# Performance work log

Hardware: AMD Instinct MI355X
Metric: run time of the kernel (lower is better)

## Reference

```python
import jax, jax.numpy as jnp
import numpy as np

B, S, V = 512, 256, 10      # batch, s_node_num, v_node_num
E, H = 128, 128             # embedding, lstm hidden
D = 2 * H                   # num_directions * hidden
PENALTY = 1.0e6
STD = 0.1


def _cell(x, h, c, Wih, Whh, b):
    # PyTorch LSTM cell, gate order i, f, g, o; b = b_ih + b_hh
    g = x @ Wih.T + h @ Whh.T + b
    i, f, gg, o = jnp.split(g, 4, axis=-1)
    c = jax.nn.sigmoid(f) * c + jax.nn.sigmoid(i) * jnp.tanh(gg)
    h = jax.nn.sigmoid(o) * jnp.tanh(c)
    return h, c


def setup_inputs() -> dict:
    key = jax.random.key(0)
    ks = jax.random.split(key, 25)
    w = lambda k, shp: (jax.random.normal(k, shp, jnp.float32) * STD)
    return {
        's_node_indexes': jax.random.randint(ks[0], (B, S), 0, S, dtype=jnp.int32),
        's_inputs': jax.random.uniform(ks[1], (B, S, 3), jnp.float32),
        'v_input': jax.random.uniform(ks[2], (V, 3), jnp.float32) * 0.5,
        'W_embed': w(ks[3], (E, 1)),
        'enc_Wih_f': w(ks[4], (4 * H, E)), 'enc_Whh_f': w(ks[5], (4 * H, H)), 'enc_b_f': w(ks[6], (4 * H,)),
        'enc_Wih_b': w(ks[7], (4 * H, E)), 'enc_Whh_b': w(ks[8], (4 * H, H)), 'enc_b_b': w(ks[9], (4 * H,)),
        'dec_Wih_f': w(ks[10], (4 * H, D)), 'dec_Whh_f': w(ks[11], (4 * H, H)), 'dec_b_f': w(ks[12], (4 * H,)),
        'dec_Wih_b': w(ks[13], (4 * H, D)), 'dec_Whh_b': w(ks[14], (4 * H, H)), 'dec_b_b': w(ks[15], (4 * H,)),
        'W_ref': w(ks[16], (D, D)), 'W_q': w(ks[17], (D, D)), 'v_w': w(ks[18], (D,)),
        'W_ref2': w(ks[19], (D, D)), 'W_q2': w(ks[20], (D, D)), 'v2_w': w(ks[21], (D,)),
    }


def reference(s_node_indexes, s_inputs, v_input, W_embed,
              enc_Wih_f, enc_Whh_f, enc_b_f, enc_Wih_b, enc_Whh_b, enc_b_b,
              dec_Wih_f, dec_Whh_f, dec_b_f, dec_Wih_b, dec_Whh_b, dec_b_b,
              W_ref, W_q, v_w, W_ref2, W_q2, v2_w):
    Bn, Sn = s_node_indexes.shape
    # Embed: snode resource -> Linear(1, E, bias=False)
    emb = s_inputs[:, :, 0:1] @ W_embed.T            # (B, S, E)
    xs = jnp.swapaxes(emb, 0, 1)                     # (S, B, E)
    h0 = jnp.zeros((Bn, H), jnp.float32)
    c0 = jnp.zeros((Bn, H), jnp.float32)

    def enc_scan(Wih, Whh, b, seq):
        def step(carry, x):
            h, c = carry
            h, c = _cell(x, h, c, Wih, Whh, b)
            return (h, c), h
        (hT, cT), hs = jax.lax.scan(step, (h0, c0), seq)
        return hs, hT, cT

    hs_f, hf, cf = enc_scan(enc_Wih_f, enc_Whh_f, enc_b_f, xs)
    hs_b, hb, cb = enc_scan(enc_Wih_b, enc_Whh_b, enc_b_b, xs[::-1])
    Enc = jnp.swapaxes(jnp.concatenate([hs_f, hs_b[::-1]], axis=-1), 0, 1)  # (B, S, D)
    h_state = jnp.stack([hf, hb])                    # (2, B, H)
    c_state = jnp.stack([cf, cb])

    refE = Enc @ W_ref.T                             # (B, S, D) precomputed (dropout p=0)
    ref2E = Enc @ W_ref2.T

    def dec_step(carry, vcpu):
        dec_in, h, c, played = carry                 # dec_in (B, D)
        hf_, cf_ = _cell(dec_in, h[0], c[0], dec_Wih_f, dec_Whh_f, dec_b_f)
        hb_, cb_ = _cell(dec_in, h[1], c[1], dec_Wih_b, dec_Whh_b, dec_b_b)
        dec_out = jnp.concatenate([hf_, hb_], axis=-1)                       # (B, D)
        cannot = (s_inputs[:, :, 0] < vcpu).astype(jnp.float32) + played     # (B, S)
        ow = jnp.tanh(refE + (dec_out @ W_q.T)[:, None, :]) @ v_w - PENALTY * cannot
        att = jax.nn.softmax(jnp.tanh(ref2E + (dec_in @ W_q2.T)[:, None, :]) @ v2_w, axis=1)
        new_in = jnp.einsum('bs,bsd->bd', att, Enc)
        sel = jnp.argmax(ow, axis=1)
        played = played + jax.nn.one_hot(sel, Sn, dtype=jnp.float32)
        return (new_in, jnp.stack([hf_, hb_]), jnp.stack([cf_, cb_]), played), (ow, sel)

    init = (jnp.zeros((Bn, D), jnp.float32), h_state, c_state, jnp.zeros((Bn, Sn), jnp.float32))
    _, (output_weights, sels) = jax.lax.scan(dec_step, init, v_input[:, 0])
    shuffled = sels.T                                # (B, V)
    original = jnp.take_along_axis(s_node_indexes, shuffled, axis=1)
    return original, shuffled, output_weights        # output_weights: (V, B, S)
```

## Files before the change

kernel.cpp:

```cpp
#include <hip/hip_runtime.h>
#include <math.h>

#define cB 512
#define cS 256
#define cV 10
#define cE 128
#define cH 128
#define cD 256
#define cG 512
#define PEN 1.0e6f
#define S1 224
#define PADK 40

typedef _Float16 half8_t __attribute__((ext_vector_type(8)));
typedef _Float16 half4_t __attribute__((ext_vector_type(4)));
typedef float f32x4 __attribute__((ext_vector_type(4)));

#define DOT4(acc, wv, hv)                                   \
    do {                                                    \
        acc = fmaf((wv).x, (hv).x, acc);                    \
        acc = fmaf((wv).y, (hv).y, acc);                    \
        acc = fmaf((wv).z, (hv).z, acc);                    \
        acc = fmaf((wv).w, (hv).w, acc);                    \
    } while (0)

__device__ __forceinline__ float sigmf(float x) { return 1.0f / (1.0f + expf(-x)); }

__global__ void k_uprep(const float* __restrict__ Wih_f, const float* __restrict__ Wih_b,
                        const float* __restrict__ W_embed, float* __restrict__ uvec)
{
    const int j = threadIdx.x;
    const float* __restrict__ Wih = blockIdx.x ? Wih_b : Wih_f;
    float u = 0.f;
#pragma unroll 8
    for (int e = 0; e < cE; ++e) u = fmaf(Wih[(size_t)j * cE + e], W_embed[e], u);
    uvec[blockIdx.x * cG + j] = u;
}

__global__ __launch_bounds__(1024, 4) void k_encoder(
    const float* __restrict__ s_inputs, const float* __restrict__ uvec,
    const float* __restrict__ Whh_f, const float* __restrict__ b_f,
    const float* __restrict__ Whh_b, const float* __restrict__ b_b,
    _Float16* __restrict__ Ehi, _Float16* __restrict__ Elo,
    float* __restrict__ h_state, float* __restrict__ c_state)
{
    const int dir = blockIdx.x >> 7;
    const int b0  = (blockIdx.x & 127) * 4;
    const float* __restrict__ Whh = dir ? Whh_b : Whh_f;
    const float* __restrict__ bv  = dir ? b_b   : b_f;
    const int tid = threadIdx.x;
    const int j = tid & 511;
    const int hf = tid >> 9;

    __shared__ __align__(16) float a_in[4][cS];
    __shared__ __align__(16) float hbuf[4][cH];
    __shared__ __align__(16) float gpart[4][2][516];

    a_in[tid >> 8][tid & 255] =
        s_inputs[((size_t)(b0 + (tid >> 8)) * cS + (tid & 255)) * 3];

    float4 w[16];
#pragma unroll
    for (int kk = 0; kk < 16; ++kk)
        w[kk] = *(const float4*)&Whh[(size_t)j * cH + hf * 64 + kk * 4];

    const float uj = (hf == 0) ? uvec[dir * cG + j] : 0.f;
    const float bj = (hf == 0) ? bv[j] : 0.f;

    const int ur = tid >> 7, uk = tid & 127;
    float c_reg = 0.f, h_last = 0.f;
    if (tid < 512) hbuf[ur][uk] = 0.f;
    __syncthreads();

    for (int p = 0; p < cS; ++p) {
        const int s = dir ? (cS - 1 - p) : p;
        float acc0 = fmaf(a_in[0][s], uj, bj);
        float acc1 = fmaf(a_in[1][s], uj, bj);
        float acc2 = fmaf(a_in[2][s], uj, bj);
        float acc3 = fmaf(a_in[3][s], uj, bj);
#pragma unroll
        for (int kk = 0; kk < 16; ++kk) {
            const float4 wv = w[kk];
            const float4 h0 = *(const float4*)&hbuf[0][hf * 64 + kk * 4];
            DOT4(acc0, wv, h0);
            const float4 h1 = *(const float4*)&hbuf[1][hf * 64 + kk * 4];
            DOT4(acc1, wv, h1);
            const float4 h2 = *(const float4*)&hbuf[2][hf * 64 + kk * 4];
            DOT4(acc2, wv, h2);
            const float4 h3 = *(const float4*)&hbuf[3][hf * 64 + kk * 4];
            DOT4(acc3, wv, h3);
        }
        gpart[0][hf][j] = acc0;
        gpart[1][hf][j] = acc1;
        gpart[2][hf][j] = acc2;
        gpart[3][hf][j] = acc3;
        __syncthreads();

        if (tid < 512) {
            const float gi = gpart[ur][0][uk]       + gpart[ur][1][uk];
            const float gf = gpart[ur][0][128 + uk] + gpart[ur][1][128 + uk];
            const float gg = gpart[ur][0][256 + uk] + gpart[ur][1][256 + uk];
            const float go = gpart[ur][0][384 + uk] + gpart[ur][1][384 + uk];
            const float i_ = sigmf(gi), f_ = sigmf(gf), g_ = tanhf(gg), o_ = sigmf(go);
            c_reg = fmaf(f_, c_reg, i_ * g_);
            const float hn = o_ * tanhf(c_reg);
            h_last = hn;
            hbuf[ur][uk] = hn;
            const size_t eidx = ((size_t)(b0 + ur) * cS + s) * cD + dir * cH + uk;
            const _Float16 hh = (_Float16)hn;
            Ehi[eidx] = hh;
            Elo[eidx] = (_Float16)(hn - (float)hh);
        }
        __syncthreads();
    }
    if (tid < 512) {
        h_state[((size_t)dir * cB + b0 + ur) * cH + uk] = h_last;
        c_state[((size_t)dir * cB + b0 + ur) * cH + uk] = c_reg;
    }
}

__global__ void k_split_w(const float* __restrict__ W1, const float* __restrict__ W2,
                          _Float16* __restrict__ Whi1, _Float16* __restrict__ Wlo1,
                          _Float16* __restrict__ Whi2, _Float16* __restrict__ Wlo2)
{
    const int i = blockIdx.x * 256 + threadIdx.x;
    {
        float a = W1[i]; _Float16 h = (_Float16)a;
        Whi1[i] = h; Wlo1[i] = (_Float16)(a - (float)h);
    }
    {
        float a = W2[i]; _Float16 h = (_Float16)a;
        Whi2[i] = h; Wlo2[i] = (_Float16)(a - (float)h);
    }
}

__global__ __launch_bounds__(256) void k_head_mat(
    const _Float16* __restrict__ Ahi, const _Float16* __restrict__ Alo,
    const _Float16* __restrict__ Whi, const _Float16* __restrict__ Wlo,
    float* __restrict__ outv)
{
    const int tid = threadIdx.x;
    const int w = tid >> 6, l = tid & 63;
    const int m0 = blockIdx.x * 64;

    __shared__ __align__(16) _Float16 As[2][64][PADK];
    __shared__ __align__(16) _Float16 Ws[2][256][PADK];

    const int r = tid >> 2, kq = tid & 3;
    size_t arow;
    {
        const int m = m0 + r;
        const int s = m >> 9, b = m & 511;
        arow = ((size_t)b * cS + s) * cD;
    }
    const size_t wrow = (size_t)tid * cD;

    f32x4 acc[16];
#pragma unroll
    for (int i = 0; i < 16; ++i) acc[i] = (f32x4){0.f, 0.f, 0.f, 0.f};

    const int fr = w * 16 + (l & 15);
    const int kc = (l >> 4) * 8;

    for (int k0 = 0; k0 < 256; k0 += 32) {
        __syncthreads();
        *(uint4*)&As[0][r][kq * 8] = *(const uint4*)&Ahi[arow + k0 + kq * 8];
        *(uint4*)&As[1][r][kq * 8] = *(const uint4*)&Alo[arow + k0 + kq * 8];
#pragma unroll
        for (int q4 = 0; q4 < 4; ++q4) {
            *(uint4*)&Ws[0][tid][q4 * 8] = *(const uint4*)&Whi[wrow + k0 + q4 * 8];
            *(uint4*)&Ws[1][tid][q4 * 8] = *(const uint4*)&Wlo[wrow + k0 + q4 * 8];
        }
        __syncthreads();

        const half8_t ahi = *(const half8_t*)&As[0][fr][kc];
        const half8_t alo = *(const half8_t*)&As[1][fr][kc];
#pragma unroll
        for (int nf = 0; nf < 16; ++nf) {
            const int n = nf * 16 + (l & 15);
            const half8_t bhi = *(const half8_t*)&Ws[0][n][kc];
            const half8_t blo = *(const half8_t*)&Ws[1][n][kc];
            acc[nf] = __builtin_amdgcn_mfma_f32_16x16x32_f16(ahi, bhi, acc[nf], 0, 0, 0);
            acc[nf] = __builtin_amdgcn_mfma_f32_16x16x32_f16(ahi, blo, acc[nf], 0, 0, 0);
            acc[nf] = __builtin_amdgcn_mfma_f32_16x16x32_f16(alo, bhi, acc[nf], 0, 0, 0);
        }
    }
#pragma unroll
    for (int nf = 0; nf < 16; ++nf)
#pragma unroll
        for (int rr = 0; rr < 4; ++rr) {
            const int m = w * 16 + ((l >> 4) << 2) + rr;
            outv[(size_t)(m0 + m) * cD + nf * 16 + (l & 15)] = acc[nf][rr];
        }
}

template <int MODE>
__global__ __launch_bounds__(512, 2) void k_head2(
    const _Float16* __restrict__ Ahi, const _Float16* __restrict__ Alo,
    const _Float16* __restrict__ Whi, const _Float16* __restrict__ Wlo,
    const float* __restrict__ qv, const float* __restrict__ vv,
    float* __restrict__ outv)
{
    const int tid = threadIdx.x;
    const int l = tid & 63;
    const int w = tid >> 6;
    const int wm = w >> 2, wn = w & 3;
    const int g = l >> 4, li = l & 15;
    const int m0 = blockIdx.x * 128;

    __shared__ __align__(16) _Float16 Ah[128][PADK];
    __shared__ __align__(16) _Float16 Al[128][PADK];
    __shared__ __align__(16) _Float16 Wh[256][PADK];
    __shared__ __align__(16) _Float16 Wl[256][PADK];
    __shared__ __align__(16) float qs[4][cD];
    __shared__ __align__(16) float vs[cD];
    __shared__ float spart[4][128];

    if (MODE == 0) {
        const int b = m0 >> 8;
        if (tid < 256) qs[0][tid] = qv[(size_t)b * cD + tid];
        else           vs[tid - 256] = vv[tid - 256];
    } else {
        const int b0 = m0 >> 5;
        qs[tid >> 8][tid & 255] = qv[(size_t)(b0 + (tid >> 8)) * cD + (tid & 255)];
        const int i2 = tid + 512;
        qs[i2 >> 8][i2 & 255] = qv[(size_t)(b0 + (i2 >> 8)) * cD + (i2 & 255)];
        if (tid < 256) vs[tid] = vv[tid];
    }

    const int ar = tid >> 2, aq = tid & 3;
    size_t arow;
    {
        const int m = m0 + ar;
        if (MODE == 0) arow = (size_t)m * cD;
        else { const int b = m >> 5, s = S1 + (m & 31); arow = ((size_t)b * cS + s) * cD; }
    }

    f32x4 acc[4][4];
#pragma unroll
    for (int mi = 0; mi < 4; ++mi)
#pragma unroll
        for (int ni = 0; ni < 4; ++ni) acc[mi][ni] = (f32x4){0.f, 0.f, 0.f, 0.f};

    for (int k0 = 0; k0 < 256; k0 += 32) {
        __syncthreads();
        *(uint4*)&Ah[ar][aq * 8] = *(const uint4*)&Ahi[arow + k0 + aq * 8];
        *(uint4*)&Al[ar][aq * 8] = *(const uint4*)&Alo[arow + k0 + aq * 8];
        *(uint4*)&Wh[ar][aq * 8] = *(const uint4*)&Whi[(size_t)ar * cD + k0 + aq * 8];
        *(uint4*)&Wl[ar][aq * 8] = *(const uint4*)&Wlo[(size_t)ar * cD + k0 + aq * 8];
        *(uint4*)&Wh[ar + 128][aq * 8] = *(const uint4*)&Whi[(size_t)(ar + 128) * cD + k0 + aq * 8];
        *(uint4*)&Wl[ar + 128][aq * 8] = *(const uint4*)&Wlo[(size_t)(ar + 128) * cD + k0 + aq * 8];
        __syncthreads();

        half8_t ah[4], al[4];
#pragma unroll
        for (int mi = 0; mi < 4; ++mi) {
            ah[mi] = *(const half8_t*)&Ah[wm * 64 + mi * 16 + li][g * 8];
            al[mi] = *(const half8_t*)&Al[wm * 64 + mi * 16 + li][g * 8];
        }
#pragma unroll
        for (int ni = 0; ni < 4; ++ni) {
            const half8_t bh = *(const half8_t*)&Wh[wn * 64 + ni * 16 + li][g * 8];
            const half8_t bl = *(const half8_t*)&Wl[wn * 64 + ni * 16 + li][g * 8];
#pragma unroll
            for (int mi = 0; mi < 4; ++mi) {
                acc[mi][ni] = __builtin_amdgcn_mfma_f32_16x16x32_f16(ah[mi], bh, acc[mi][ni], 0, 0, 0);
                acc[mi][ni] = __builtin_amdgcn_mfma_f32_16x16x32_f16(ah[mi], bl, acc[mi][ni], 0, 0, 0);
                acc[mi][ni] = __builtin_amdgcn_mfma_f32_16x16x32_f16(al[mi], bh, acc[mi][ni], 0, 0, 0);
            }
        }
    }

    float val = 0.f;
#pragma unroll
    for (int mi = 0; mi < 4; ++mi)
#pragma unroll
        for (int rr = 0; rr < 4; ++rr) {
            const int row = wm * 64 + mi * 16 + g * 4 + rr;
            const int bl = (MODE == 1) ? (row >> 5) : 0;
            float p = 0.f;
#pragma unroll
            for (int ni = 0; ni < 4; ++ni) {
                const int c = wn * 64 + ni * 16 + li;
                p = fmaf(vs[c], tanhf(acc[mi][ni][rr] + qs[bl][c]), p);
            }
            p += __shfl_xor(p, 1);
            p += __shfl_xor(p, 2);
            p += __shfl_xor(p, 4);
            p += __shfl_xor(p, 8);
            if (li == mi * 4 + rr) val = p;
        }
    {
        const int row_out = wm * 64 + (li >> 2) * 16 + g * 4 + (li & 3);
        spart[wn][row_out] = val;
    }
    __syncthreads();
    if (tid < 128)
        outv[m0 + tid] = spart[0][tid] + spart[1][tid] + spart[2][tid] + spart[3][tid];
}

__global__ __launch_bounds__(256, 4) void k_fold(
    const float* __restrict__ refC, const float* __restrict__ q1v,
    const float* __restrict__ v_w, float* __restrict__ sc1lo)
{
    const int tid = threadIdx.x;
    const int m0 = blockIdx.x * 64;
    const int r = tid >> 2, p = tid & 3;
    const int m = m0 + r;
    const int b = m & 511;
    __shared__ float red[64][4];

    const float* row  = refC + (size_t)m * cD + p * 64;
    const float* qrow = q1v + (size_t)b * cD + p * 64;
    const float* vrow = v_w + p * 64;
    float s = 0.f;
#pragma unroll 4
    for (int d = 0; d < 64; d += 4) {
        const float4 rv4 = *(const float4*)&row[d];
        const float4 q4  = *(const float4*)&qrow[d];
        const float4 v4  = *(const float4*)&vrow[d];
        s = fmaf(v4.x, tanhf(rv4.x + q4.x), s);
        s = fmaf(v4.y, tanhf(rv4.y + q4.y), s);
        s = fmaf(v4.z, tanhf(rv4.z + q4.z), s);
        s = fmaf(v4.w, tanhf(rv4.w + q4.w), s);
    }
    red[r][p] = s;
    __syncthreads();
    if (tid < 64)
        sc1lo[m0 + tid] = red[tid][0] + red[tid][1] + red[tid][2] + red[tid][3];
}

__global__ __launch_bounds__(512, 2) void k_dec_cells(
    const float* __restrict__ dec_in,
    const float* __restrict__ Wih_f, const float* __restrict__ Whh_f, const float* __restrict__ b_f,
    const float* __restrict__ Wih_b, const float* __restrict__ Whh_b, const float* __restrict__ b_b,
    float* __restrict__ h_state, float* __restrict__ c_state, float* __restrict__ dec_out)
{
    const int cell = blockIdx.x >> 7;
    const int b0 = (blockIdx.x & 127) * 4;
    const float* __restrict__ Wih = cell ? Wih_b : Wih_f;
    const float* __restrict__ Whh = cell ? Whh_b : Whh_f;
    const float* __restrict__ bv  = cell ? b_b   : b_f;
    const int j = threadIdx.x;

    __shared__ __align__(16) float xin[4][cD];
    __shared__ __align__(16) float hin[4][cH];
    __shared__ __align__(16) float gbuf[4][cG];

    for (int idx = j; idx < 4 * cD; idx += 512) {
        int bb = idx >> 8, k = idx & 255;
        xin[bb][k] = dec_in[(size_t)(b0 + bb) * cD + k];
    }
    {
        int bb = j >> 7, k = j & 127;
        hin[bb][k] = h_state[((size_t)cell * cB + b0 + bb) * cH + k];
    }
    __syncthreads();

    float a0 = bv[j];
    float a1 = a0, a2 = a0, a3 = a0;
#pragma unroll 4
    for (int kk = 0; kk < 64; ++kk) {
        const float4 wv = *(const float4*)&Wih[(size_t)j * cD + kk * 4];
        const float4 x0 = *(const float4*)&xin[0][kk * 4]; DOT4(a0, wv, x0);
        const float4 x1 = *(const float4*)&xin[1][kk * 4]; DOT4(a1, wv, x1);
        const float4 x2 = *(const float4*)&xin[2][kk * 4]; DOT4(a2, wv, x2);
        const float4 x3 = *(const float4*)&xin[3][kk * 4]; DOT4(a3, wv, x3);
    }
#pragma unroll 4
    for (int kk = 0; kk < 32; ++kk) {
        const float4 wv = *(const float4*)&Whh[(size_t)j * cH + kk * 4];
        const float4 h0 = *(const float4*)&hin[0][kk * 4]; DOT4(a0, wv, h0);
        const float4 h1 = *(const float4*)&hin[1][kk * 4]; DOT4(a1, wv, h1);
        const float4 h2 = *(const float4*)&hin[2][kk * 4]; DOT4(a2, wv, h2);
        const float4 h3 = *(const float4*)&hin[3][kk * 4]; DOT4(a3, wv, h3);
    }
    gbuf[0][j] = a0; gbuf[1][j] = a1; gbuf[2][j] = a2; gbuf[3][j] = a3;
    __syncthreads();

    const int uk = j & 127, ub = j >> 7;
    const float gi = gbuf[ub][uk];
    const float gf = gbuf[ub][128 + uk];
    const float gg = gbuf[ub][256 + uk];
    const float go = gbuf[ub][384 + uk];
    const size_t sidx = ((size_t)cell * cB + b0 + ub) * cH + uk;
    const float c_old = c_state[sidx];
    const float i_ = sigmf(gi), f_ = sigmf(gf), g_ = tanhf(gg), o_ = sigmf(go);
    const float cn = fmaf(f_, c_old, i_ * g_);
    const float hn = o_ * tanhf(cn);
    c_state[sidx] = cn;
    h_state[sidx] = hn;
    dec_out[(size_t)(b0 + ub) * cD + cell * cH + uk] = hn;
}

__global__ __launch_bounds__(256, 2) void k_qproj(
    const float* __restrict__ dec_out, const float* __restrict__ dec_in_old,
    const float* __restrict__ W_q, const float* __restrict__ W_q2,
    float* __restrict__ q1v, float* __restrict__ q2v)
{
    const int b = blockIdx.x;
    const int tid = threadIdx.x;
    __shared__ __align__(16) float dout[cD];
    __shared__ __align__(16) float din[cD];
    dout[tid] = dec_out[(size_t)b * cD + tid];
    din[tid]  = dec_in_old[(size_t)b * cD + tid];
    __syncthreads();
    float s1 = 0.0f, s2 = 0.0f;
#pragma unroll 4
    for (int kk = 0; kk < 64; ++kk) {
        const float4 w1 = *(const float4*)&W_q[(size_t)tid * cD + kk * 4];
        const float4 w2 = *(const float4*)&W_q2[(size_t)tid * cD + kk * 4];
        const float4 x1 = *(const float4*)&dout[kk * 4];
        const float4 x2 = *(const float4*)&din[kk * 4];
        DOT4(s1, w1, x1);
        DOT4(s2, w2, x2);
    }
    q1v[(size_t)b * cD + tid] = s1;
    q2v[(size_t)b * cD + tid] = s2;
}

__global__ __launch_bounds__(256, 2) void k_finish(
    const float* __restrict__ sc1lo, const float* __restrict__ sc1hi,
    const float* __restrict__ sc2,
    const _Float16* __restrict__ Ehi, const _Float16* __restrict__ Elo,
    const float* __restrict__ s_inputs, const int* __restrict__ s_node_indexes,
    const float* __restrict__ v_input, float* __restrict__ played,
    float* __restrict__ dec_in_new, float* __restrict__ outp, int t)
{
    const int b = blockIdx.x;
    const int tid = threadIdx.x;
    const int lane = tid & 63;
    const int wv = tid >> 6;

    __shared__ __align__(16) float atr[cS];
    __shared__ __align__(16) float part[4][cD];
    __shared__ float rv[cS];
    __shared__ int   ri[cS];

    const float owv = (tid < S1) ? sc1lo[(size_t)tid * cB + b]
                                 : sc1hi[(size_t)b * (cS - S1) + (tid - S1)];
    atr[tid] = sc2[(size_t)b * cS + tid];

    const float vcpu = v_input[t * 3];
    float val;
    {
        const float a0 = s_inputs[((size_t)b * cS + tid) * 3];
        const float can = (a0 < vcpu ? 1.0f : 0.0f) + played[(size_t)b * cS + tid];
        val = owv - PEN * can;
        outp[2 * cB * cV + ((size_t)t * cB + b) * cS + tid] = val;
    }
    rv[tid] = val; ri[tid] = tid;
    __syncthreads();
#pragma unroll
    for (int off = 128; off > 0; off >>= 1) {
        if (tid < off) {
            const float v2 = rv[tid + off]; const int i2 = ri[tid + off];
            const float v1 = rv[tid];       const int i1 = ri[tid];
            if (v2 > v1 || (v2 == v1 && i2 < i1)) { rv[tid] = v2; ri[tid] = i2; }
        }
        __syncthreads();
    }
    const int sel = ri[0];
    __syncthreads();
    if (tid == 0) {
        played[(size_t)b * cS + sel] += 1.0f;
        outp[(size_t)b * cV + t] = (float)s_node_indexes[(size_t)b * cS + sel];
        outp[(size_t)cB * cV + (size_t)b * cV + t] = (float)sel;
    }

    rv[tid] = atr[tid];
    __syncthreads();
#pragma unroll
    for (int off = 128; off > 0; off >>= 1) {
        if (tid < off) { const float v2 = rv[tid + off]; if (v2 > rv[tid]) rv[tid] = v2; }
        __syncthreads();
    }
    const float mx = rv[0];
    __syncthreads();
    const float ex = expf(atr[tid] - mx);
    rv[tid] = ex;
    __syncthreads();
#pragma unroll
    for (int off = 128; off > 0; off >>= 1) {
        if (tid < off) rv[tid] += rv[tid + off];
        __syncthreads();
    }
    const float ssum = rv[0];
    __syncthreads();
    atr[tid] = ex / ssum;
    __syncthreads();

    {
        float4 acc = make_float4(0.f, 0.f, 0.f, 0.f);
        for (int s2i = wv * 64; s2i < wv * 64 + 64; ++s2i) {
            const float a = atr[s2i];
            const size_t eidx = ((size_t)b * cS + s2i) * cD + lane * 4;
            const half4_t h4 = *(const half4_t*)&Ehi[eidx];
            const half4_t l4 = *(const half4_t*)&Elo[eidx];
            acc.x = fmaf(a, (float)h4[0] + (float)l4[0], acc.x);
            acc.y = fmaf(a, (float)h4[1] + (float)l4[1], acc.y);
            acc.z = fmaf(a, (float)h4[2] + (float)l4[2], acc.z);
            acc.w = fmaf(a, (float)h4[3] + (float)l4[3], acc.w);
        }
        *(float4*)&part[wv][lane * 4] = acc;
    }
    __syncthreads();
    dec_in_new[(size_t)b * cD + tid] =
        part[0][tid] + part[1][tid] + part[2][tid] + part[3][tid];
}

extern "C" void kernel_launch(void* const* d_in, const int* in_sizes, int n_in,
                              void* d_out, int out_size, void* d_ws, size_t ws_size,
                              hipStream_t stream)
{
    (void)in_sizes; (void)n_in; (void)out_size; (void)ws_size;

    const int*   s_node = (const int*)  d_in[0];
    const float* s_inp  = (const float*)d_in[1];
    const float* v_inp  = (const float*)d_in[2];
    const float* W_emb  = (const float*)d_in[3];
    const float* eWih_f = (const float*)d_in[4];
    const float* eWhh_f = (const float*)d_in[5];
    const float* eb_f   = (const float*)d_in[6];
    const float* eWih_b = (const float*)d_in[7];
    const float* eWhh_b = (const float*)d_in[8];
    const float* eb_b   = (const float*)d_in[9];
    const float* dWih_f = (const float*)d_in[10];
    const float* dWhh_f = (const float*)d_in[11];
    const float* db_f   = (const float*)d_in[12];
    const float* dWih_b = (const float*)d_in[13];
    const float* dWhh_b = (const float*)d_in[14];
    const float* db_b   = (const float*)d_in[15];
    const float* W_ref  = (const float*)d_in[16];
    const float* W_q    = (const float*)d_in[17];
    const float* v_w    = (const float*)d_in[18];
    const float* W_ref2 = (const float*)d_in[19];
    const float* W_q2   = (const float*)d_in[20];
    const float* v2_w   = (const float*)d_in[21];

    float* out = (float*)d_out;
    const size_t ENCSZ = (size_t)cB * cS * cD;
    const size_t SMALL = (size_t)cB * cD;

    char* p = (char*)d_ws;
    _Float16* Ehi = (_Float16*)p; p += ENCSZ * 2;
    _Float16* Elo = (_Float16*)p; p += ENCSZ * 2;
    float* refC  = (float*)p;     p += (size_t)S1 * cB * cD * 4;
    _Float16* Whi1 = (_Float16*)p; p += (size_t)cD * cD * 2;
    _Float16* Wlo1 = (_Float16*)p; p += (size_t)cD * cD * 2;
    _Float16* Whi2 = (_Float16*)p; p += (size_t)cD * cD * 2;
    _Float16* Wlo2 = (_Float16*)p; p += (size_t)cD * cD * 2;
    float* hst    = (float*)p; p += SMALL * 4;
    float* cst    = (float*)p; p += SMALL * 4;
    float* din0   = (float*)p; p += SMALL * 4;
    float* din1   = (float*)p; p += SMALL * 4;
    float* doutb  = (float*)p; p += SMALL * 4;
    float* played = (float*)p; p += SMALL * 4;
    float* q1v    = (float*)p; p += SMALL * 4;
    float* q2v    = (float*)p; p += SMALL * 4;
    float* sc2    = (float*)p; p += SMALL * 4;
    float* sc1lo  = (float*)p; p += (size_t)S1 * cB * 4;
    float* sc1hi  = (float*)p; p += (size_t)(cS - S1) * cB * 4;
    float* uvec   = (float*)p; p += 2 * cG * 4;

    hipMemsetAsync(played, 0, SMALL * sizeof(float), stream);
    hipMemsetAsync(din0,   0, SMALL * sizeof(float), stream);

    k_split_w<<<256, 256, 0, stream>>>(W_ref, W_ref2, Whi1, Wlo1, Whi2, Wlo2);
    k_uprep<<<2, 512, 0, stream>>>(eWih_f, eWih_b, W_emb, uvec);

    k_encoder<<<256, 1024, 0, stream>>>(s_inp, uvec, eWhh_f, eb_f, eWhh_b, eb_b,
                                        Ehi, Elo, hst, cst);

    k_head_mat<<<(S1 * cB) / 64, 256, 0, stream>>>(Ehi, Elo, Whi1, Wlo1, refC);

    for (int t = 0; t < cV; ++t) {
        float* di_old = (t & 1) ? din1 : din0;
        float* di_new = (t & 1) ? din0 : din1;
        k_dec_cells<<<256, 512, 0, stream>>>(di_old, dWih_f, dWhh_f, db_f,
                                             dWih_b, dWhh_b, db_b, hst, cst, doutb);
        k_qproj<<<512, 256, 0, stream>>>(doutb, di_old, W_q, W_q2, q1v, q2v);
        k_head2<0><<<(cB * cS) / 128, 512, 0, stream>>>(Ehi, Elo, Whi2, Wlo2,
                                                        q2v, v2_w, sc2);
        k_head2<1><<<(cB * (cS - S1)) / 128, 512, 0, stream>>>(Ehi, Elo, Whi1, Wlo1,
                                                               q1v, v_w, sc1hi);
        k_fold<<<(S1 * cB) / 64, 256, 0, stream>>>(refC, q1v, v_w, sc1lo);

        k_finish<<<512, 256, 0, stream>>>(sc1lo, sc1hi, sc2, Ehi, Elo,
                                          s_inp, s_node, v_inp, played, di_new, out, t);
    }
}
```

Measured before the change: 3.468 ms.

## Rebalance precomputed vs recomputed attention heads and fuse scoring into one kernel

Both attention heads are now split into a precomputed part, where the ref projection is stored once after the encoder, and a part recomputed each step with MFMA. The split points are 112/144 for the output head and 128/128 for the glimpse head. The three per-step scoring kernels (head2<0>, head2<1>, fold) become one k_score launch that dispatches on block index, cutting launch count and letting the MFMA and fold work overlap. In exchange the precompute grows by 128 extra rows for the second head, which adds one-time workspace and compute. The per-row q1v global loads in the MFMA epilogue may also cost bandwidth.

```diff
diff --git a/kernel.cpp b/kernel.cpp
--- a/kernel.cpp
+++ b/kernel.cpp
@@ -9,8 +9,11 @@
 #define cD 256
 #define cG 512
 #define PEN 1.0e6f
-#define S1 224
 #define PADK 40
+#define S1OW 112
+#define L1OW 144
+#define S2AT 128
+#define L2AT 128
 
 typedef _Float16 half8_t __attribute__((ext_vector_type(8)));
 typedef _Float16 half4_t __attribute__((ext_vector_type(4)));
@@ -74,26 +77,20 @@
 
     for (int p = 0; p < cS; ++p) {
         const int s = dir ? (cS - 1 - p) : p;
-        float acc0 = fmaf(a_in[0][s], uj, bj);
-        float acc1 = fmaf(a_in[1][s], uj, bj);
-        float acc2 = fmaf(a_in[2][s], uj, bj);
-        float acc3 = fmaf(a_in[3][s], uj, bj);
+        float a0[4];
+#pragma unroll
+        for (int r = 0; r < 4; ++r) a0[r] = fmaf(a_in[r][s], uj, bj);
 #pragma unroll
         for (int kk = 0; kk < 16; ++kk) {
             const float4 wv = w[kk];
-            const float4 h0 = *(const float4*)&hbuf[0][hf * 64 + kk * 4];
-            DOT4(acc0, wv, h0);
-            const float4 h1 = *(const float4*)&hbuf[1][hf * 64 + kk * 4];
-            DOT4(acc1, wv, h1);
-            const float4 h2 = *(const float4*)&hbuf[2][hf * 64 + kk * 4];
-            DOT4(acc2, wv, h2);
-            const float4 h3 = *(const float4*)&hbuf[3][hf * 64 + kk * 4];
-            DOT4(acc3, wv, h3);
-        }
-        gpart[0][hf][j] = acc0;
-        gpart[1][hf][j] = acc1;
-        gpart[2][hf][j] = acc2;
-        gpart[3][hf][j] = acc3;
+#pragma unroll
+            for (int r = 0; r < 4; ++r) {
+                const float4 h4 = *(const float4*)&hbuf[r][hf * 64 + kk * 4];
+                DOT4(a0[r], wv, h4);
+            }
+        }
+#pragma unroll
+        for (int r = 0; r < 4; ++r) gpart[r][hf][j] = a0[r];
         __syncthreads();
 
         if (tid < 512) {
@@ -134,14 +131,21 @@
     }
 }
 
-__global__ __launch_bounds__(256) void k_head_mat(
+__global__ __launch_bounds__(256) void k_head_mat2(
     const _Float16* __restrict__ Ahi, const _Float16* __restrict__ Alo,
-    const _Float16* __restrict__ Whi, const _Float16* __restrict__ Wlo,
-    float* __restrict__ outv)
-{
+    const _Float16* __restrict__ Whi1, const _Float16* __restrict__ Wlo1,
+    const _Float16* __restrict__ Whi2, const _Float16* __restrict__ Wlo2,
+    float* __restrict__ refC, float* __restrict__ ref2C)
+{
+    const int blk = blockIdx.x;
+    const bool is1 = blk < (S1OW * cB / 64);
+    const _Float16* __restrict__ Whi = is1 ? Whi1 : Whi2;
+    const _Float16* __restrict__ Wlo = is1 ? Wlo1 : Wlo2;
+    float* __restrict__ outv = is1 ? refC : ref2C;
+    const int m0 = (is1 ? blk : blk - S1OW * cB / 64) * 64;
+
     const int tid = threadIdx.x;
     const int w = tid >> 6, l = tid & 63;
-    const int m0 = blockIdx.x * 64;
 
     __shared__ __align__(16) _Float16 As[2][64][PADK];
     __shared__ __align__(16) _Float16 Ws[2][256][PADK];
@@ -194,140 +198,156 @@
         }
 }
 
-template <int MODE>
-__global__ __launch_bounds__(512, 2) void k_head2(
+__global__ __launch_bounds__(512, 2) void k_score(
     const _Float16* __restrict__ Ahi, const _Float16* __restrict__ Alo,
-    const _Float16* __restrict__ Whi, const _Float16* __restrict__ Wlo,
-    const float* __restrict__ qv, const float* __restrict__ vv,
-    float* __restrict__ outv)
-{
+    const _Float16* __restrict__ Whi1, const _Float16* __restrict__ Wlo1,
+    const _Float16* __restrict__ Whi2, const _Float16* __restrict__ Wlo2,
+    const float* __restrict__ refC, const float* __restrict__ ref2C,
+    const float* __restrict__ q1v, const float* __restrict__ q2v,
+    const float* __restrict__ v_w, const float* __restrict__ v2_w,
+    float* __restrict__ sc1lo, float* __restrict__ sc1hi,
+    float* __restrict__ sc2lo, float* __restrict__ sc2hi)
+{
+    __shared__ __align__(16) char smem[65536];
+    const int blk = blockIdx.x;
     const int tid = threadIdx.x;
-    const int l = tid & 63;
-    const int w = tid >> 6;
-    const int wm = w >> 2, wn = w & 3;
-    const int g = l >> 4, li = l & 15;
-    const int m0 = blockIdx.x * 128;
-
-    __shared__ __align__(16) _Float16 Ah[128][PADK];
-    __shared__ __align__(16) _Float16 Al[128][PADK];
-    __shared__ __align__(16) _Float16 Wh[256][PADK];
-    __shared__ __align__(16) _Float16 Wl[256][PADK];
-    __shared__ __align__(16) float qs[4][cD];
-    __shared__ __align__(16) float vs[cD];
-    __shared__ float spart[4][128];
-
-    if (MODE == 0) {
-        const int b = m0 >> 8;
-        if (tid < 256) qs[0][tid] = qv[(size_t)b * cD + tid];
-        else           vs[tid - 256] = vv[tid - 256];
+
+    if (blk < 1088) {
+        const bool isow = blk < 576;
+        const _Float16* __restrict__ Whi = isow ? Whi1 : Whi2;
+        const _Float16* __restrict__ Wlo = isow ? Wlo1 : Wlo2;
+        const int batt = blk - 576;
+        const int m0 = isow ? blk * 128 : 0;
+
+        _Float16 (*Ah)[PADK] = (_Float16(*)[PADK])(smem);
+        _Float16 (*Al)[PADK] = (_Float16(*)[PADK])(smem + 10240);
+        _Float16 (*Wh)[PADK] = (_Float16(*)[PADK])(smem + 20480);
+        _Float16 (*Wl)[PADK] = (_Float16(*)[PADK])(smem + 40960);
+        float* qs = (float*)(smem + 61440);
+        float* vs = (float*)(smem + 62464);
+        float (*spart)[128] = (float(*)[128])(smem + 63488);
+
+        const int l = tid & 63;
+        const int w = tid >> 6;
+        const int wm = w >> 2, wn = w & 3;
+        const int g = l >> 4, li = l & 15;
+
+        if (isow) {
+            if (tid < 256) vs[tid] = v_w[tid];
+        } else {
+            if (tid < 256) qs[tid] = q2v[(size_t)batt * cD + tid];
+            else           vs[tid - 256] = v2_w[tid - 256];
+        }
+
+        const int ar = tid >> 2, aq = tid & 3;
+        size_t arow;
+        if (isow) {
+            const int m = m0 + ar;
+            const int bq = m / L1OW;
+            const int s = S1OW + (m - bq * L1OW);
+            arow = ((size_t)bq * cS + s) * cD;
+        } else {
+            arow = ((size_t)batt * cS + S2AT + ar) * cD;
+        }
+
+        f32x4 acc[4][4];
+#pragma unroll
+        for (int mi = 0; mi < 4; ++mi)
+#pragma unroll
+            for (int ni = 0; ni < 4; ++ni) acc[mi][ni] = (f32x4){0.f, 0.f, 0.f, 0.f};
+
+        for (int k0 = 0; k0 < 256; k0 += 32) {
+            __syncthreads();
+            *(uint4*)&Ah[ar][aq * 8] = *(const uint4*)&Ahi[arow + k0 + aq * 8];
+            *(uint4*)&Al[ar][aq * 8] = *(const uint4*)&Alo[arow + k0 + aq * 8];
+            *(uint4*)&Wh[ar][aq * 8] = *(const uint4*)&Whi[(size_t)ar * cD + k0 + aq * 8];
+            *(uint4*)&Wl[ar][aq * 8] = *(const uint4*)&Wlo[(size_t)ar * cD + k0 + aq * 8];
+            *(uint4*)&Wh[ar + 128][aq * 8] = *(const uint4*)&Whi[(size_t)(ar + 128) * cD + k0 + aq * 8];
+            *(uint4*)&Wl[ar + 128][aq * 8] = *(const uint4*)&Wlo[(size_t)(ar + 128) * cD + k0 + aq * 8];
+            __syncthreads();
+
+            half8_t ah[4], al[4];
+#pragma unroll
+            for (int mi = 0; mi < 4; ++mi) {
+                ah[mi] = *(const half8_t*)&Ah[wm * 64 + mi * 16 + li][g * 8];
+                al[mi] = *(const half8_t*)&Al[wm * 64 + mi * 16 + li][g * 8];
+            }
+#pragma unroll
+            for (int ni = 0; ni < 4; ++ni) {
+                const half8_t bh = *(const half8_t*)&Wh[wn * 64 + ni * 16 + li][g * 8];
+                const half8_t bl = *(const half8_t*)&Wl[wn * 64 + ni * 16 + li][g * 8];
+#pragma unroll
+                for (int mi = 0; mi < 4; ++mi) {
+                    acc[mi][ni] = __builtin_amdgcn_mfma_f32_16x16x32_f16(ah[mi], bh, acc[mi][ni], 0, 0, 0);
+                    acc[mi][ni] = __builtin_amdgcn_mfma_f32_16x16x32_f16(ah[mi], bl, acc[mi][ni], 0, 0, 0);
+                    acc[mi][ni] = __builtin_amdgcn_mfma_f32_16x16x32_f16(al[mi], bh, acc[mi][ni], 0, 0, 0);
+                }
+            }
+        }
+
+        float val = 0.f;
+#pragma unroll
+        for (int mi = 0; mi < 4; ++mi)
+#pragma unroll
+            for (int rr = 0; rr < 4; ++rr) {
+                const int row = wm * 64 + mi * 16 + g * 4 + rr;
+                float p = 0.f;
+#pragma unroll
+                for (int ni = 0; ni < 4; ++ni) {
+                    const int c = wn * 64 + ni * 16 + li;
+                    const float qq = isow ? q1v[(size_t)((m0 + row) / L1OW) * cD + c]
+                                          : qs[c];
+                    p = fmaf(vs[c], tanhf(acc[mi][ni][rr] + qq), p);
+                }
+                p += __shfl_xor(p, 1);
+                p += __shfl_xor(p, 2);
+                p += __shfl_xor(p, 4);
+                p += __shfl_xor(p, 8);
+                if (li == mi * 4 + rr) val = p;
+            }
+        {
+            const int row_out = wm * 64 + (li >> 2) * 16 + g * 4 + (li & 3);
+            spart[wn][row_out] = val;
+        }
+        __syncthreads();
+        if (tid < 128) {
+            const float o = spart[0][tid] + spart[1][tid] + spart[2][tid] + spart[3][tid];
+            if (isow) sc1hi[m0 + tid] = o;
+            else      sc2hi[(size_t)batt * L2AT + tid] = o;
+        }
     } else {
-        const int b0 = m0 >> 5;
-        qs[tid >> 8][tid & 255] = qv[(size_t)(b0 + (tid >> 8)) * cD + (tid & 255)];
-        const int i2 = tid + 512;
-        qs[i2 >> 8][i2 & 255] = qv[(size_t)(b0 + (i2 >> 8)) * cD + (i2 & 255)];
-        if (tid < 256) vs[tid] = vv[tid];
-    }
-
-    const int ar = tid >> 2, aq = tid & 3;
-    size_t arow;
-    {
-        const int m = m0 + ar;
-        if (MODE == 0) arow = (size_t)m * cD;
-        else { const int b = m >> 5, s = S1 + (m & 31); arow = ((size_t)b * cS + s) * cD; }
-    }
-
-    f32x4 acc[4][4];
-#pragma unroll
-    for (int mi = 0; mi < 4; ++mi)
-#pragma unroll
-        for (int ni = 0; ni < 4; ++ni) acc[mi][ni] = (f32x4){0.f, 0.f, 0.f, 0.f};
-
-    for (int k0 = 0; k0 < 256; k0 += 32) {
-        __syncthreads();
-        *(uint4*)&Ah[ar][aq * 8] = *(const uint4*)&Ahi[arow + k0 + aq * 8];
-        *(uint4*)&Al[ar][aq * 8] = *(const uint4*)&Alo[arow + k0 + aq * 8];
-        *(uint4*)&Wh[ar][aq * 8] = *(const uint4*)&Whi[(size_t)ar * cD + k0 + aq * 8];
-        *(uint4*)&Wl[ar][aq * 8] = *(const uint4*)&Wlo[(size_t)ar * cD + k0 + aq * 8];
-        *(uint4*)&Wh[ar + 128][aq * 8] = *(const uint4*)&Whi[(size_t)(ar + 128) * cD + k0 + aq * 8];
-        *(uint4*)&Wl[ar + 128][aq * 8] = *(const uint4*)&Wlo[(size_t)(ar + 128) * cD + k0 + aq * 8];
-        __syncthreads();
-
-        half8_t ah[4], al[4];
-#pragma unroll
-        for (int mi = 0; mi < 4; ++mi) {
-            ah[mi] = *(const half8_t*)&Ah[wm * 64 + mi * 16 + li][g * 8];
-            al[mi] = *(const half8_t*)&Al[wm * 64 + mi * 16 + li][g * 8];
-        }
-#pragma unroll
-        for (int ni = 0; ni < 4; ++ni) {
-            const half8_t bh = *(const half8_t*)&Wh[wn * 64 + ni * 16 + li][g * 8];
-            const half8_t bl = *(const half8_t*)&Wl[wn * 64 + ni * 16 + li][g * 8];
-#pragma unroll
-            for (int mi = 0; mi < 4; ++mi) {
-                acc[mi][ni] = __builtin_amdgcn_mfma_f32_16x16x32_f16(ah[mi], bh, acc[mi][ni], 0, 0, 0);
-                acc[mi][ni] = __builtin_amdgcn_mfma_f32_16x16x32_f16(ah[mi], bl, acc[mi][ni], 0, 0, 0);
-                acc[mi][ni] = __builtin_amdgcn_mfma_f32_16x16x32_f16(al[mi], bh, acc[mi][ni], 0, 0, 0);
-            }
-        }
-    }
-
-    float val = 0.f;
-#pragma unroll
-    for (int mi = 0; mi < 4; ++mi)
-#pragma unroll
-        for (int rr = 0; rr < 4; ++rr) {
-            const int row = wm * 64 + mi * 16 + g * 4 + rr;
-            const int bl = (MODE == 1) ? (row >> 5) : 0;
-            float p = 0.f;
-#pragma unroll
-            for (int ni = 0; ni < 4; ++ni) {
-                const int c = wn * 64 + ni * 16 + li;
-                p = fmaf(vs[c], tanhf(acc[mi][ni][rr] + qs[bl][c]), p);
-            }
-            p += __shfl_xor(p, 1);
-            p += __shfl_xor(p, 2);
-            p += __shfl_xor(p, 4);
-            p += __shfl_xor(p, 8);
-            if (li == mi * 4 + rr) val = p;
-        }
-    {
-        const int row_out = wm * 64 + (li >> 2) * 16 + g * 4 + (li & 3);
-        spart[wn][row_out] = val;
-    }
-    __syncthreads();
-    if (tid < 128)
-        outv[m0 + tid] = spart[0][tid] + spart[1][tid] + spart[2][tid] + spart[3][tid];
-}
-
-__global__ __launch_bounds__(256, 4) void k_fold(
-    const float* __restrict__ refC, const float* __restrict__ q1v,
-    const float* __restrict__ v_w, float* __restrict__ sc1lo)
-{
-    const int tid = threadIdx.x;
-    const int m0 = blockIdx.x * 64;
-    const int r = tid >> 2, p = tid & 3;
-    const int m = m0 + r;
-    const int b = m & 511;
-    __shared__ float red[64][4];
-
-    const float* row  = refC + (size_t)m * cD + p * 64;
-    const float* qrow = q1v + (size_t)b * cD + p * 64;
-    const float* vrow = v_w + p * 64;
-    float s = 0.f;
+        const int fb = blk - 1088;
+        const bool isowf = fb < 448;
+        const float* __restrict__ C  = isowf ? refC : ref2C;
+        const float* __restrict__ qv = isowf ? q1v : q2v;
+        const float* __restrict__ vv = isowf ? v_w : v2_w;
+        float* __restrict__ outv     = isowf ? sc1lo : sc2lo;
+        const int m0 = (isowf ? fb : fb - 448) * 128;
+
+        float (*red)[4] = (float(*)[4])smem;
+        const int r = tid >> 2, p2 = tid & 3;
+        const int m = m0 + r;
+        const int b = m & 511;
+
+        const float* row  = C + (size_t)m * cD + p2 * 64;
+        const float* qrow = qv + (size_t)b * cD + p2 * 64;
+        const float* vrow = vv + p2 * 64;
+        float s = 0.f;
 #pragma unroll 4
-    for (int d = 0; d < 64; d += 4) {
-        const float4 rv4 = *(const float4*)&row[d];
-        const float4 q4  = *(const float4*)&qrow[d];
-        const float4 v4  = *(const float4*)&vrow[d];
-        s = fmaf(v4.x, tanhf(rv4.x + q4.x), s);
-        s = fmaf(v4.y, tanhf(rv4.y + q4.y), s);
-        s = fmaf(v4.z, tanhf(rv4.z + q4.z), s);
-        s = fmaf(v4.w, tanhf(rv4.w + q4.w), s);
-    }
-    red[r][p] = s;
-    __syncthreads();
-    if (tid < 64)
-        sc1lo[m0 + tid] = red[tid][0] + red[tid][1] + red[tid][2] + red[tid][3];
+        for (int d = 0; d < 64; d += 4) {
+            const float4 rv4 = *(const float4*)&row[d];
+            const float4 q4  = *(const float4*)&qrow[d];
+            const float4 v4  = *(const float4*)&vrow[d];
+            s = fmaf(v4.x, tanhf(rv4.x + q4.x), s);
+            s = fmaf(v4.y, tanhf(rv4.y + q4.y), s);
+            s = fmaf(v4.z, tanhf(rv4.z + q4.z), s);
+            s = fmaf(v4.w, tanhf(rv4.w + q4.w), s);
+        }
+        red[r][p2] = s;
+        __syncthreads();
+        if (tid < 128)
+            outv[m0 + tid] = red[tid][0] + red[tid][1] + red[tid][2] + red[tid][3];
+    }
 }
 
 __global__ __launch_bounds__(512, 2) void k_dec_cells(
@@ -421,7 +441,7 @@
 
 __global__ __launch_bounds__(256, 2) void k_finish(
     const float* __restrict__ sc1lo, const float* __restrict__ sc1hi,
-    const float* __restrict__ sc2,
+    const float* __restrict__ sc2lo, const float* __restrict__ sc2hi,
     const _Float16* __restrict__ Ehi, const _Float16* __restrict__ Elo,
     const float* __restrict__ s_inputs, const int* __restrict__ s_node_indexes,
     const float* __restrict__ v_input, float* __restrict__ played,
@@ -437,9 +457,10 @@
     __shared__ float rv[cS];
     __shared__ int   ri[cS];
 
-    const float owv = (tid < S1) ? sc1lo[(size_t)tid * cB + b]
-                                 : sc1hi[(size_t)b * (cS - S1) + (tid - S1)];
-    atr[tid] = sc2[(size_t)b * cS + tid];
+    const float owv = (tid < S1OW) ? sc1lo[(size_t)tid * cB + b]
+                                   : sc1hi[(size_t)b * L1OW + (tid - S1OW)];
+    atr[tid] = (tid < S2AT) ? sc2lo[(size_t)tid * cB + b]
+                            : sc2hi[(size_t)b * L2AT + (tid - S2AT)];
 
     const float vcpu = v_input[t * 3];
     float val;
@@ -543,9 +564,10 @@
     const size_t SMALL = (size_t)cB * cD;
 
     char* p = (char*)d_ws;
-    _Float16* Ehi = (_Float16*)p; p += ENCSZ * 2;
-    _Float16* Elo = (_Float16*)p; p += ENCSZ * 2;
-    float* refC  = (float*)p;     p += (size_t)S1 * cB * cD * 4;
+    _Float16* Ehi  = (_Float16*)p; p += ENCSZ * 2;
+    _Float16* Elo  = (_Float16*)p; p += ENCSZ * 2;
+    float* refC    = (float*)p;    p += (size_t)S1OW * cB * cD * 4;
+    float* ref2C   = (float*)p;    p += (size_t)S2AT * cB * cD * 4;
     _Float16* Whi1 = (_Float16*)p; p += (size_t)cD * cD * 2;
     _Float16* Wlo1 = (_Float16*)p; p += (size_t)cD * cD * 2;
     _Float16* Whi2 = (_Float16*)p; p += (size_t)cD * cD * 2;
@@ -558,9 +580,10 @@
     float* played = (float*)p; p += SMALL * 4;
     float* q1v    = (float*)p; p += SMALL * 4;
     float* q2v    = (float*)p; p += SMALL * 4;
-    float* sc2    = (float*)p; p += SMALL * 4;
-    float* sc1lo  = (float*)p; p += (size_t)S1 * cB * 4;
-    float* sc1hi  = (float*)p; p += (size_t)(cS - S1) * cB * 4;
+    float* sc1lo  = (float*)p; p += (size_t)S1OW * cB * 4;
+    float* sc1hi  = (float*)p; p += (size_t)L1OW * cB * 4;
+    float* sc2lo  = (float*)p; p += (size_t)S2AT * cB * 4;
+    float* sc2hi  = (float*)p; p += (size_t)L2AT * cB * 4;
     float* uvec   = (float*)p; p += 2 * cG * 4;
 
     hipMemsetAsync(played, 0, SMALL * sizeof(float), stream);
@@ -572,7 +595,8 @@
     k_encoder<<<256, 1024, 0, stream>>>(s_inp, uvec, eWhh_f, eb_f, eWhh_b, eb_b,
                                         Ehi, Elo, hst, cst);
 
-    k_head_mat<<<(S1 * cB) / 64, 256, 0, stream>>>(Ehi, Elo, Whi1, Wlo1, refC);
+    k_head_mat2<<<(S1OW + S2AT) * cB / 64, 256, 0, stream>>>(
+        Ehi, Elo, Whi1, Wlo1, Whi2, Wlo2, refC, ref2C);
 
     for (int t = 0; t < cV; ++t) {
         float* di_old = (t & 1) ? din1 : din0;
@@ -580,13 +604,10 @@
         k_dec_cells<<<256, 512, 0, stream>>>(di_old, dWih_f, dWhh_f, db_f,
                                              dWih_b, dWhh_b, db_b, hst, cst, doutb);
         k_qproj<<<512, 256, 0, stream>>>(doutb, di_old, W_q, W_q2, q1v, q2v);
-        k_head2<0><<<(cB * cS) / 128, 512, 0, stream>>>(Ehi, Elo, Whi2, Wlo2,
-                                                        q2v, v2_w, sc2);
-        k_head2<1><<<(cB * (cS - S1)) / 128, 512, 0, stream>>>(Ehi, Elo, Whi1, Wlo1,
-                                                               q1v, v_w, sc1hi);
-        k_fold<<<(S1 * cB) / 64, 256, 0, stream>>>(refC, q1v, v_w, sc1lo);
-
-        k_finish<<<512, 256, 0, stream>>>(sc1lo, sc1hi, sc2, Ehi, Elo,
+        k_score<<<2048, 512, 0, stream>>>(Ehi, Elo, Whi1, Wlo1, Whi2, Wlo2,
+                                          refC, ref2C, q1v, q2v, v_w, v2_w,
+                                          sc1lo, sc1hi, sc2lo, sc2hi);
+        k_finish<<<512, 256, 0, stream>>>(sc1lo, sc1hi, sc2lo, sc2hi, Ehi, Elo,
                                           s_inp, s_node, v_inp, played, di_new, out, t);
     }
 }
```

Result: faster. 3.119 ms (-10.1%).
